# Kernel tuning notes

Hardware: AMD Instinct MI355X
Metric: run time of the kernel (lower is better)

## Reference

```python
import jax, jax.numpy as jnp
import numpy as np

TEMPERATURE = 0.07
N_ANCHORS = 256
THRESHOLD = 0.1
EPS_VALID = 1e-6


def setup_inputs() -> dict:
    key = jax.random.key(0)
    kf, kp, ka = jax.random.split(key, 3)
    B, N, D, H, W = 8, 4, 256, 48, 64
    HW = H * W
    # channels-first features, as the module's permute branch expects
    features = jax.random.normal(kf, (B, N, D, H, W), dtype=jnp.float32)
    # uniform[0,1) -> all points valid (norm > 1e-6) and NN dists mostly < threshold
    pointmaps = jax.random.uniform(kp, (B, N, H, W, 3), dtype=jnp.float32)
    # deterministic stand-in for torch.randperm(N_i)[:n_anchors], one per (view pair, batch)
    keys = jax.random.split(ka, (N - 1) * B)
    perm = jax.vmap(lambda k: jax.random.permutation(k, HW)[:N_ANCHORS])(keys)
    anchor_idx = perm.reshape(N - 1, B, N_ANCHORS).astype(jnp.int32)
    return {"features": features, "pointmaps": pointmaps, "anchor_idx": anchor_idx}


def _l2norm(x):
    # F.normalize(dim=-1) semantics
    return x / jnp.clip(jnp.linalg.norm(x, axis=-1, keepdims=True), 1e-12)


def _pair_loss(fi, fj, pi, pj, vi, vj, aidx):
    # fi, fj: [HW, D]; pi, pj: [HW, 3]; vi, vj: [HW] bool; aidx: [A]
    a_pts = pi[aidx]                                   # [A, 3]
    a_feats = fi[aidx]                                 # [A, D]
    # cdist(anchor_pts, pts_j): [A, HW]
    d2 = jnp.sum((a_pts[:, None, :] - pj[None, :, :]) ** 2, axis=-1)
    dists = jnp.sqrt(jnp.maximum(d2, 0.0))
    dists = jnp.where(vj[None, :], dists, jnp.inf)     # invalid j points can't be matched
    pos_idx = jnp.argmin(dists, axis=-1)               # [A]
    min_d = jnp.min(dists, axis=-1)                    # [A]
    valid_a = (min_d < THRESHOLD) & vi[aidx]           # anchor must be valid + matched
    a_n = _l2norm(a_feats)                             # [A, D]
    p_n = _l2norm(fj[pos_idx])                         # [A, D]
    all_n = _l2norm(fj)                                # [HW, D]
    pos_sim = jnp.sum(a_n * p_n, axis=-1) / TEMPERATURE            # [A]
    all_sim = jnp.einsum('ad,jd->aj', a_n, all_n) / TEMPERATURE    # [A, HW]
    all_sim = jnp.where(vj[None, :], all_sim, -jnp.inf)            # mask invalid negatives
    loss_a = -pos_sim + jax.nn.logsumexp(all_sim, axis=-1)         # [A]
    cnt = jnp.sum(valid_a)
    loss_b = jnp.sum(jnp.where(valid_a, loss_a, 0.0)) / jnp.maximum(cnt, 1)
    include = (cnt >= 5) & (jnp.sum(vi) >= 10) & (jnp.sum(vj) >= 10)
    return loss_b, include


def reference(features, pointmaps, anchor_idx):
    if features.shape[-1] != features.shape[-2]:
        features = jnp.transpose(features, (0, 1, 3, 4, 2))  # [B,N,D,H,W] -> [B,N,H,W,D]
    B, N, H, W, D = features.shape
    feats = features.reshape(B, N, H * W, D)
    pts = pointmaps.reshape(B, N, H * W, 3)
    valid = jnp.linalg.norm(pts, axis=-1) > EPS_VALID    # [B, N, HW]
    total = jnp.float32(0.0)
    for v in range(1, N):  # small fixed loop over view pairs (0, v)
        lb, inc = jax.vmap(_pair_loss)(
            feats[:, 0], feats[:, v], pts[:, 0], pts[:, v],
            valid[:, 0], valid[:, v], anchor_idx[v - 1])
        n_inc = jnp.sum(inc)
        pair = jnp.where(n_inc > 0,
                         jnp.sum(jnp.where(inc, lb, 0.0)) / jnp.maximum(n_inc, 1),
                         0.0)
        total = total + pair
    return total / max(N - 1, 1)
```

## Files before the change

### kernel.cpp

```cpp
#include <hip/hip_runtime.h>
#include <math.h>

#define B_ 8
#define N_ 4
#define D_ 256
#define HW_ 3072
#define A_ 256
#define NP_ 3
#define NJT2_ 48
#define NJB_ 96
#define INV_T 14.2857142857142857f
#define LDKH 64

typedef _Float16 half8 __attribute__((ext_vector_type(8)));
typedef _Float16 half2v __attribute__((ext_vector_type(2)));
typedef float f32x4 __attribute__((ext_vector_type(4)));
typedef unsigned uint2v __attribute__((ext_vector_type(2)));

__global__ __launch_bounds__(256) void k_prep_nn(const float* __restrict__ f,
        const float* __restrict__ pts, _Float16* __restrict__ fh,
        float* __restrict__ srn_g,
        unsigned char* __restrict__ valid, int* __restrict__ vcnt_part,
        const int* __restrict__ aidx, int* __restrict__ pos_idx,
        unsigned char* __restrict__ valid_a, int* __restrict__ ticket) {
  __shared__ float ssql[4][8][4];
  int tid = threadIdx.x;

  if (blockIdx.x < 96) {
    int j0 = blockIdx.x * 32;
    int bn = blockIdx.y;
    int n = bn & 3;
    int jq = tid & 7;
    int dr = (tid >> 3) & 15;
    int hh = tid >> 7;

    f32x4 rv[2][4];
#pragma unroll
    for (int dtl = 0; dtl < 2; ++dtl) {
      int dt = 2 * hh + dtl;
      const float* fb = f + ((size_t)bn * D_ + dt * 64 + 4 * dr) * HW_ + j0 + 4 * jq;
      rv[dtl][0] = *(const f32x4*)&fb[0];
      rv[dtl][1] = *(const f32x4*)&fb[HW_];
      rv[dtl][2] = *(const f32x4*)&fb[2 * HW_];
      rv[dtl][3] = *(const f32x4*)&fb[3 * HW_];
    }

#pragma unroll
    for (int dtl = 0; dtl < 2; ++dtl) {
      int dt = 2 * hh + dtl;
      f32x4 r0 = rv[dtl][0], r1 = rv[dtl][1], r2 = rv[dtl][2], r3 = rv[dtl][3];
#pragma unroll
      for (int jj = 0; jj < 4; ++jj) {
        half2v a, b2;
        a[0]  = (_Float16)r0[jj]; a[1]  = (_Float16)r1[jj];
        b2[0] = (_Float16)r2[jj]; b2[1] = (_Float16)r3[jj];
        uint2v w;
        w[0] = __builtin_bit_cast(unsigned, a);
        w[1] = __builtin_bit_cast(unsigned, b2);
        *(uint2v*)&fh[((size_t)bn * HW_ + j0 + 4 * jq + jj) * D_ + dt * 64 + 4 * dr] = w;
      }
    }

    float ssq0 = 0.f, ssq1 = 0.f, ssq2 = 0.f, ssq3 = 0.f;
#pragma unroll
    for (int dtl = 0; dtl < 2; ++dtl) {
      f32x4 r0 = rv[dtl][0], r1 = rv[dtl][1], r2 = rv[dtl][2], r3 = rv[dtl][3];
      ssq0 = fmaf(r0[0], r0[0], fmaf(r1[0], r1[0], fmaf(r2[0], r2[0], fmaf(r3[0], r3[0], ssq0))));
      ssq1 = fmaf(r0[1], r0[1], fmaf(r1[1], r1[1], fmaf(r2[1], r2[1], fmaf(r3[1], r3[1], ssq1))));
      ssq2 = fmaf(r0[2], r0[2], fmaf(r1[2], r1[2], fmaf(r2[2], r2[2], fmaf(r3[2], r3[2], ssq2))));
      ssq3 = fmaf(r0[3], r0[3], fmaf(r1[3], r1[3], fmaf(r2[3], r2[3], fmaf(r3[3], r3[3], ssq3))));
    }
    ssq0 += __shfl_xor(ssq0, 8); ssq0 += __shfl_xor(ssq0, 16); ssq0 += __shfl_xor(ssq0, 32);
    ssq1 += __shfl_xor(ssq1, 8); ssq1 += __shfl_xor(ssq1, 16); ssq1 += __shfl_xor(ssq1, 32);
    ssq2 += __shfl_xor(ssq2, 8); ssq2 += __shfl_xor(ssq2, 16); ssq2 += __shfl_xor(ssq2, 32);
    ssq3 += __shfl_xor(ssq3, 8); ssq3 += __shfl_xor(ssq3, 16); ssq3 += __shfl_xor(ssq3, 32);
    if ((tid & 63) < 8) {
      int w = tid >> 6;
      ssql[w][jq][0] = ssq0; ssql[w][jq][1] = ssq1;
      ssql[w][jq][2] = ssq2; ssql[w][jq][3] = ssq3;
    }
    __syncthreads();
    if (tid < 32) {
      float s = ssql[0][tid >> 2][tid & 3] + ssql[1][tid >> 2][tid & 3]
              + ssql[2][tid >> 2][tid & 3] + ssql[3][tid >> 2][tid & 3];
      float r = 1.f / fmaxf(sqrtf(s), 1e-12f);
      size_t idx = (size_t)bn * HW_ + j0 + tid;
      srn_g[idx] = (n == 0) ? r * INV_T : r;
      const float* p = pts + idx * 3;
      float x = p[0], y = p[1], z = p[2];
      int v = (x * x + y * y + z * z) > 1e-12f ? 1 : 0;
      valid[idx] = (unsigned char)v;
      unsigned long long mask = __ballot(v);
      if (tid == 0) vcnt_part[bn * NJB_ + blockIdx.x] = __popcll(mask);
    }
  } else {
    int gid = (blockIdx.x - 96) * 32 + blockIdx.y;
    if (gid == 0 && tid == 0) *ticket = 0;
    int wave = tid >> 6, lane = tid & 63;
    int agrp = gid & 63;
    int b = (gid >> 6) & 7;
    int p = gid >> 9;
    int a = agrp * 4 + wave;
    int vv = p + 1;
    int col = aidx[(p * B_ + b) * A_ + a];
    const float* pi = pts + ((size_t)(b * N_) * HW_ + col) * 3;
    float ax = pi[0], ay = pi[1], az = pi[2];
    int vi = (ax * ax + ay * ay + az * az) > 1e-12f ? 1 : 0;
    const f32x4* pj4 = (const f32x4*)(pts + (size_t)(b * N_ + vv) * HW_ * 3);
    float best = INFINITY; int bidx = 0x7fffffff;
#pragma unroll 2
    for (int t = 0; t < HW_ / 256; ++t) {
      int jb = t * 256 + lane * 4;
      int base = t * 192 + lane * 3;
      f32x4 q0 = pj4[base + 0];
      f32x4 q1 = pj4[base + 1];
      f32x4 q2 = pj4[base + 2];
      float px[4] = {q0[0], q0[3], q1[2], q2[1]};
      float py[4] = {q0[1], q1[0], q1[3], q2[2]};
      float pz[4] = {q0[2], q1[1], q2[0], q2[3]};
#pragma unroll
      for (int k = 0; k < 4; ++k) {
        float x = px[k], y = py[k], z = pz[k];
        int vj = (x * x + y * y + z * z) > 1e-12f;
        float dx = ax - x, dy = ay - y, dz = az - z;
        float dist = sqrtf(dx * dx + dy * dy + dz * dz);
        int j = jb + k;
        if (vj && (dist < best || (dist == best && j < bidx))) { best = dist; bidx = j; }
      }
    }
#pragma unroll
    for (int o = 32; o > 0; o >>= 1) {
      float ob = __shfl_xor(best, o);
      int oi = __shfl_xor(bidx, o);
      if (ob < best || (ob == best && oi < bidx)) { best = ob; bidx = oi; }
    }
    if (lane == 0) {
      int ai = (p * B_ + b) * A_ + a;
      pos_idx[ai] = (bidx == 0x7fffffff) ? 0 : bidx;
      valid_a[ai] = (best < 0.1f) && vi;
    }
  }
}

#define STAGE_AB(KK, BUF) do {                                                 \
  _Pragma("unroll")                                                            \
  for (int cc = 0; cc < 4; ++cc) {                                             \
    const _Float16* srcA = fA + (size_t)colA[cc] * D_ + (KK) * 64 + gsw * 8;   \
    __builtin_amdgcn_global_load_lds(                                          \
        (const __attribute__((address_space(1))) void*)srcA,                   \
        (__attribute__((address_space(3))) void*)&As[BUF][(wid * 32 + cc * 8) * LDKH], \
        16, 0, 0);                                                             \
  }                                                                            \
  _Pragma("unroll")                                                            \
  for (int cc = 0; cc < 4; ++cc) {                                             \
    const _Float16* srcB = fB + (size_t)rowB[cc] * D_ + (KK) * 64 + gsw * 8;   \
    __builtin_amdgcn_global_load_lds(                                          \
        (const __attribute__((address_space(1))) void*)srcB,                   \
        (__attribute__((address_space(3))) void*)&Bs[BUF][(wid * 32 + cc * 8) * LDKH], \
        16, 0, 0);                                                             \
  }                                                                            \
} while (0)

__global__ __launch_bounds__(256) void k_gemm(const _Float16* __restrict__ fh,
    const float* __restrict__ srn_g, const int* __restrict__ aidx,
    const unsigned char* __restrict__ valid, const int* __restrict__ pos_idx,
    float* __restrict__ possim, float2* __restrict__ partials) {
  __shared__ __align__(16) char smem[65536];
  _Float16 (*As)[128 * LDKH] = reinterpret_cast<_Float16 (*)[128 * LDKH]>(smem);
  _Float16 (*Bs)[128 * LDKH] = reinterpret_cast<_Float16 (*)[128 * LDKH]>(smem + 32768);
  float (*scr)[132] = reinterpret_cast<float (*)[132]>(smem);

  int jt = blockIdx.x;
  int pbm = blockIdx.y;
  int pb = pbm >> 1, mt = pbm & 1;
  int b = pb & 7, p = pb >> 3, v = p + 1;
  int tid = threadIdx.x;
  int wid = tid >> 6, lane = tid & 63;
  int wr = wid >> 1, wc = wid & 1;
  int j0 = jt * 128;
  const _Float16* fA = fh + (size_t)(b * N_) * HW_ * D_;
  const _Float16* fB = fh + (size_t)(b * N_ + v) * HW_ * D_;

  int rl = lane >> 3;
  int gl = lane & 7;
  int gsw = gl ^ rl;
  int colA[4];
#pragma unroll
  for (int c = 0; c < 4; ++c)
    colA[c] = aidx[(p * B_ + b) * A_ + mt * 128 + wid * 32 + c * 8 + rl];
  int rowB[4];
#pragma unroll
  for (int c = 0; c < 4; ++c) rowB[c] = j0 + wid * 32 + c * 8 + rl;

  f32x4 acc[4][4];
#pragma unroll
  for (int m = 0; m < 4; ++m)
#pragma unroll
    for (int n = 0; n < 4; ++n) acc[m][n] = (f32x4)0.f;

  int kg = lane >> 4;
  int fr = lane & 15;

  STAGE_AB(0, 0);
  __syncthreads();

#pragma unroll
  for (int kk = 0; kk < 4; ++kk) {
    const int cur = kk & 1;
    if (kk < 3) STAGE_AB(kk + 1, cur ^ 1);
#pragma unroll
    for (int s = 0; s < 2; ++s) {
      half8 af[4], bf[4];
      int G = s * 4 + kg;
#pragma unroll
      for (int m = 0; m < 4; ++m) {
        int row = wr * 64 + m * 16 + fr;
        af[m] = *(half8*)&As[cur][row * LDKH + ((G ^ (row & 7)) << 3)];
      }
#pragma unroll
      for (int n = 0; n < 4; ++n) {
        int row = wc * 64 + n * 16 + fr;
        bf[n] = *(half8*)&Bs[cur][row * LDKH + ((G ^ (row & 7)) << 3)];
      }
      __builtin_amdgcn_s_setprio(1);
#pragma unroll
      for (int m = 0; m < 4; ++m)
#pragma unroll
        for (int n = 0; n < 4; ++n)
          acc[m][n] = __builtin_amdgcn_mfma_f32_16x16x32_f16(af[m], bf[n], acc[m][n], 0, 0, 0);
      __builtin_amdgcn_s_setprio(0);
    }
    if (kk < 3) __syncthreads();
  }

  __syncthreads();

  int vrow = b * N_ + v;
  int a_loc = tid >> 1, h = tid & 1;
  int aig = pb * A_ + mt * 128 + a_loc;
  int pidx = pos_idx[aig];
  int colAe = aidx[(p * B_ + b) * A_ + mt * 128 + a_loc];
  float sA = srn_g[(size_t)(b * N_) * HW_ + colAe];

#pragma unroll
  for (int pss = 0; pss < 2; ++pss) {
    if (wc == pss) {
#pragma unroll
      for (int m = 0; m < 4; ++m)
#pragma unroll
        for (int n = 0; n < 4; ++n)
          *(f32x4*)&scr[n * 16 + fr][wr * 64 + m * 16 + kg * 4] = acc[m][n];
    }
    __syncthreads();
    int jbase = j0 + pss * 64 + h * 32;
    const unsigned* vp = (const unsigned*)(valid + (size_t)vrow * HW_ + jbase);
    unsigned vw[8];
#pragma unroll
    for (int w = 0; w < 8; ++w) vw[w] = vp[w];
    float sB[32];
#pragma unroll
    for (int q4 = 0; q4 < 8; ++q4)
      *(f32x4*)&sB[q4 * 4] = *(const f32x4*)&srn_g[(size_t)vrow * HW_ + jbase + q4 * 4];
    float vv[32];
#pragma unroll
    for (int jj = 0; jj < 32; ++jj)
      vv[jj] = scr[h * 32 + jj][a_loc] * sA * sB[jj];
    float mx = -INFINITY;
#pragma unroll
    for (int jj = 0; jj < 32; ++jj) {
      if ((vw[jj >> 2] >> ((jj & 3) * 8)) & 0xff) mx = fmaxf(mx, vv[jj]);
      if (jbase + jj == pidx) possim[aig] = vv[jj];
    }
    float S = 0.f;
#pragma unroll
    for (int jj = 0; jj < 32; ++jj) {
      if ((vw[jj >> 2] >> ((jj & 3) * 8)) & 0xff) S += __expf(vv[jj] - mx);
    }
    float am = fmaxf(mx, __shfl_xor(mx, 1));
    float Ss = (mx == am) ? S : S * __expf(mx - am);
    Ss += __shfl_xor(Ss, 1);
    if (h == 0) partials[(size_t)aig * NJT2_ + (jt * 2 + pss)] = make_float2(am, Ss);
    __syncthreads();
  }
}

__global__ __launch_bounds__(1024) void k_merge(const float2* __restrict__ partials,
    const float* __restrict__ possim, const unsigned char* __restrict__ valid_a,
    const int* __restrict__ vcnt_part, float* __restrict__ lossb,
    int* __restrict__ incb, int* __restrict__ ticket, float* __restrict__ out) {
  int pb = blockIdx.x;
  int b = pb & 7, p = pb >> 3;
  int tid = threadIdx.x;
  int a = tid >> 2, q = tid & 3;
  int ai = pb * A_ + a;

  __shared__ float ss[16]; __shared__ int sc[16];
  __shared__ int v0c, vvc;
  if (tid == 0) { v0c = 0; vvc = 0; }
  __syncthreads();
  if (tid < NJB_) atomicAdd(&v0c, vcnt_part[(b * N_ + 0) * NJB_ + tid]);
  else if (tid < 2 * NJB_) atomicAdd(&vvc, vcnt_part[(b * N_ + p + 1) * NJB_ + (tid - NJB_)]);

  const float4* pt = (const float4*)partials + (size_t)ai * 24 + q * 6;
  float4 vv4[6];
#pragma unroll
  for (int i = 0; i < 6; ++i) vv4[i] = pt[i];
  float mx = -INFINITY;
#pragma unroll
  for (int i = 0; i < 6; ++i) { mx = fmaxf(mx, vv4[i].x); mx = fmaxf(mx, vv4[i].z); }
  float S = 0.f;
  if (mx != -INFINITY) {
#pragma unroll
    for (int i = 0; i < 6; ++i) {
      S += vv4[i].y * __expf(vv4[i].x - mx);
      S += vv4[i].w * __expf(vv4[i].z - mx);
    }
  }
  float am = mx;
#pragma unroll
  for (int o = 1; o < 4; o <<= 1) am = fmaxf(am, __shfl_xor(am, o));
  float Sg = S * ((mx == am) ? 1.f : __expf(mx - am));
#pragma unroll
  for (int o = 1; o < 4; o <<= 1) Sg += __shfl_xor(Sg, o);

  float contrib = 0.f; int cnt = 0;
  if (q == 0) {
    float lse = (am == -INFINITY) ? -INFINITY : am + logf(Sg);
    if (valid_a[ai]) { contrib = lse - possim[ai]; cnt = 1; }
  }
#pragma unroll
  for (int o = 4; o < 64; o <<= 1) {
    contrib += __shfl_xor(contrib, o);
    cnt += __shfl_xor(cnt, o);
  }
  if ((tid & 63) == 0) { ss[tid >> 6] = contrib; sc[tid >> 6] = cnt; }
  __syncthreads();
  if (tid == 0) {
    float s = 0.f; int c = 0;
#pragma unroll
    for (int i = 0; i < 16; ++i) { s += ss[i]; c += sc[i]; }
    float lb = s / (float)(c > 1 ? c : 1);
    int inc = (c >= 5) && (v0c >= 10) && (vvc >= 10);
    lossb[pb] = lb;
    incb[pb] = inc;
    __threadfence();
    int old = atomicAdd(ticket, 1);
    if (old == NP_ * B_ - 1) {
      __threadfence();
      float total = 0.f;
      for (int pp = 0; pp < NP_; ++pp) {
        float sacc = 0.f; int n = 0;
        for (int bb = 0; bb < B_; ++bb)
          if (incb[pp * B_ + bb]) { sacc += lossb[pp * B_ + bb]; ++n; }
        total += (n > 0) ? sacc / (float)n : 0.f;
      }
      out[0] = total / (float)NP_;
    }
  }
}

extern "C" void kernel_launch(void* const* d_in, const int* in_sizes, int n_in,
                              void* d_out, int out_size, void* d_ws, size_t ws_size,
                              hipStream_t stream) {
  const float* f   = (const float*)d_in[0];
  const float* pts = (const float*)d_in[1];
  const int* aidx  = (const int*)d_in[2];
  float* out = (float*)d_out;

  char* ws = (char*)d_ws;
  _Float16* fh          = (_Float16*)(ws);
  unsigned char* valid  = (unsigned char*)(ws + 50331648);
  int* pos_idx          = (int*)(ws + 50429952);
  unsigned char* valid_a= (unsigned char*)(ws + 50454528);
  float* possim         = (float*)(ws + 50460672);
  float* lossb          = (float*)(ws + 50485248);
  int* incb             = (int*)(ws + 50485376);
  float2* partials      = (float2*)(ws + 50485504);
  int* vcnt_part        = (int*)(ws + 52844800);
  int* ticket           = (int*)(ws + 52857088);
  float* srn_g          = (float*)(ws + 52857216);

  k_prep_nn<<<dim3(144, 32), 256, 0, stream>>>(f, pts, fh, srn_g, valid, vcnt_part,
                                               aidx, pos_idx, valid_a, ticket);
  k_gemm<<<dim3(24, NP_ * B_ * 2), 256, 0, stream>>>(fh, srn_g, aidx, valid, pos_idx,
                                                     possim, partials);
  k_merge<<<NP_ * B_, 1024, 0, stream>>>(partials, possim, valid_a, vcnt_part, lossb, incb, ticket, out);
}
```

Before: 89.03 us.

## Transpose features through swizzled LDS slab with async loads and atomic norm accumulation

The prep kernel now stages a 64-channel by 256-pixel fp32 tile into LDS with direct global-to-LDS loads, using an XOR swizzle. Each thread then reads one pixel's column, converts it to fp16 and writes 128-byte contiguous rows of the transposed feature buffer. Squared norms are accumulated across channel blocks with float atomics into a zeroed buffer, and the reciprocal norm is computed later in the GEMM epilogue. This aims for wider, more coalesced stores and fewer blocks. The cost is an extra memset, atomics, and per-element sqrt/reciprocal work in the GEMM epilogue.

```diff
diff --git a/kernel.cpp b/kernel.cpp
--- a/kernel.cpp
+++ b/kernel.cpp
@@ -8,93 +8,75 @@
 #define A_ 256
 #define NP_ 3
 #define NJT2_ 48
-#define NJB_ 96
+#define NJB_ 12
 #define INV_T 14.2857142857142857f
 #define LDKH 64
 
 typedef _Float16 half8 __attribute__((ext_vector_type(8)));
 typedef _Float16 half2v __attribute__((ext_vector_type(2)));
 typedef float f32x4 __attribute__((ext_vector_type(4)));
-typedef unsigned uint2v __attribute__((ext_vector_type(2)));
+typedef unsigned uint4v __attribute__((ext_vector_type(4)));
 
 __global__ __launch_bounds__(256) void k_prep_nn(const float* __restrict__ f,
         const float* __restrict__ pts, _Float16* __restrict__ fh,
-        float* __restrict__ srn_g,
+        float* __restrict__ ssq_g,
         unsigned char* __restrict__ valid, int* __restrict__ vcnt_part,
         const int* __restrict__ aidx, int* __restrict__ pos_idx,
         unsigned char* __restrict__ valid_a, int* __restrict__ ticket) {
-  __shared__ float ssql[4][8][4];
+  __shared__ __align__(16) float slab[64 * 256];
   int tid = threadIdx.x;
 
-  if (blockIdx.x < 96) {
-    int j0 = blockIdx.x * 32;
+  if (blockIdx.x < 48) {
+    int jt = blockIdx.x >> 2;
+    int dt = blockIdx.x & 3;
     int bn = blockIdx.y;
-    int n = bn & 3;
-    int jq = tid & 7;
-    int dr = (tid >> 3) & 15;
-    int hh = tid >> 7;
-
-    f32x4 rv[2][4];
-#pragma unroll
-    for (int dtl = 0; dtl < 2; ++dtl) {
-      int dt = 2 * hh + dtl;
-      const float* fb = f + ((size_t)bn * D_ + dt * 64 + 4 * dr) * HW_ + j0 + 4 * jq;
-      rv[dtl][0] = *(const f32x4*)&fb[0];
-      rv[dtl][1] = *(const f32x4*)&fb[HW_];
-      rv[dtl][2] = *(const f32x4*)&fb[2 * HW_];
-      rv[dtl][3] = *(const f32x4*)&fb[3 * HW_];
-    }
-
-#pragma unroll
-    for (int dtl = 0; dtl < 2; ++dtl) {
-      int dt = 2 * hh + dtl;
-      f32x4 r0 = rv[dtl][0], r1 = rv[dtl][1], r2 = rv[dtl][2], r3 = rv[dtl][3];
-#pragma unroll
-      for (int jj = 0; jj < 4; ++jj) {
-        half2v a, b2;
-        a[0]  = (_Float16)r0[jj]; a[1]  = (_Float16)r1[jj];
-        b2[0] = (_Float16)r2[jj]; b2[1] = (_Float16)r3[jj];
-        uint2v w;
-        w[0] = __builtin_bit_cast(unsigned, a);
-        w[1] = __builtin_bit_cast(unsigned, b2);
-        *(uint2v*)&fh[((size_t)bn * HW_ + j0 + 4 * jq + jj) * D_ + dt * 64 + 4 * dr] = w;
-      }
-    }
-
-    float ssq0 = 0.f, ssq1 = 0.f, ssq2 = 0.f, ssq3 = 0.f;
-#pragma unroll
-    for (int dtl = 0; dtl < 2; ++dtl) {
-      f32x4 r0 = rv[dtl][0], r1 = rv[dtl][1], r2 = rv[dtl][2], r3 = rv[dtl][3];
-      ssq0 = fmaf(r0[0], r0[0], fmaf(r1[0], r1[0], fmaf(r2[0], r2[0], fmaf(r3[0], r3[0], ssq0))));
-      ssq1 = fmaf(r0[1], r0[1], fmaf(r1[1], r1[1], fmaf(r2[1], r2[1], fmaf(r3[1], r3[1], ssq1))));
-      ssq2 = fmaf(r0[2], r0[2], fmaf(r1[2], r1[2], fmaf(r2[2], r2[2], fmaf(r3[2], r3[2], ssq2))));
-      ssq3 = fmaf(r0[3], r0[3], fmaf(r1[3], r1[3], fmaf(r2[3], r2[3], fmaf(r3[3], r3[3], ssq3))));
-    }
-    ssq0 += __shfl_xor(ssq0, 8); ssq0 += __shfl_xor(ssq0, 16); ssq0 += __shfl_xor(ssq0, 32);
-    ssq1 += __shfl_xor(ssq1, 8); ssq1 += __shfl_xor(ssq1, 16); ssq1 += __shfl_xor(ssq1, 32);
-    ssq2 += __shfl_xor(ssq2, 8); ssq2 += __shfl_xor(ssq2, 16); ssq2 += __shfl_xor(ssq2, 32);
-    ssq3 += __shfl_xor(ssq3, 8); ssq3 += __shfl_xor(ssq3, 16); ssq3 += __shfl_xor(ssq3, 32);
-    if ((tid & 63) < 8) {
-      int w = tid >> 6;
-      ssql[w][jq][0] = ssq0; ssql[w][jq][1] = ssq1;
-      ssql[w][jq][2] = ssq2; ssql[w][jq][3] = ssq3;
+    int wid = tid >> 6, lane = tid & 63;
+
+#pragma unroll
+    for (int i = 0; i < 16; ++i) {
+      int r = wid * 16 + i;
+      const float* src = f + ((size_t)bn * D_ + dt * 64 + r) * HW_
+                         + jt * 256 + ((lane ^ (r & 7)) << 2);
+      __builtin_amdgcn_global_load_lds(
+          (const __attribute__((address_space(1))) void*)src,
+          (__attribute__((address_space(3))) void*)&slab[r * 256],
+          16, 0, 0);
     }
     __syncthreads();
-    if (tid < 32) {
-      float s = ssql[0][tid >> 2][tid & 3] + ssql[1][tid >> 2][tid & 3]
-              + ssql[2][tid >> 2][tid & 3] + ssql[3][tid >> 2][tid & 3];
-      float r = 1.f / fmaxf(sqrtf(s), 1e-12f);
-      size_t idx = (size_t)bn * HW_ + j0 + tid;
-      srn_g[idx] = (n == 0) ? r * INV_T : r;
-      const float* p = pts + idx * 3;
+
+    int j = tid;
+    int gj = j >> 2, jo = j & 3;
+    float ssq = 0.f;
+    unsigned pack[32];
+#pragma unroll
+    for (int r2 = 0; r2 < 32; ++r2) {
+      int r0 = 2 * r2, r1 = 2 * r2 + 1;
+      float v0 = slab[r0 * 256 + ((gj ^ (r0 & 7)) << 2) + jo];
+      float v1 = slab[r1 * 256 + ((gj ^ (r1 & 7)) << 2) + jo];
+      ssq = fmaf(v0, v0, ssq);
+      ssq = fmaf(v1, v1, ssq);
+      half2v h;
+      h[0] = (_Float16)v0; h[1] = (_Float16)v1;
+      pack[r2] = __builtin_bit_cast(unsigned, h);
+    }
+    size_t jg = (size_t)bn * HW_ + jt * 256 + j;
+    atomicAdd(&ssq_g[jg], ssq);
+    unsigned* outw = (unsigned*)fh;
+    size_t rb = jg * (D_ / 2) + dt * 32;
+#pragma unroll
+    for (int q = 0; q < 8; ++q)
+      *(uint4v*)&outw[rb + q * 4] = *(uint4v*)&pack[q * 4];
+
+    if (dt == 0) {
+      const float* p = pts + jg * 3;
       float x = p[0], y = p[1], z = p[2];
       int v = (x * x + y * y + z * z) > 1e-12f ? 1 : 0;
-      valid[idx] = (unsigned char)v;
+      valid[jg] = (unsigned char)v;
       unsigned long long mask = __ballot(v);
-      if (tid == 0) vcnt_part[bn * NJB_ + blockIdx.x] = __popcll(mask);
+      if (lane == 0) atomicAdd(&vcnt_part[bn * NJB_ + jt], __popcll(mask));
     }
   } else {
-    int gid = (blockIdx.x - 96) * 32 + blockIdx.y;
+    int gid = (blockIdx.x - 48) * 32 + blockIdx.y;
     if (gid == 0 && tid == 0) *ticket = 0;
     int wave = tid >> 6, lane = tid & 63;
     int agrp = gid & 63;
@@ -124,8 +106,8 @@
         int vj = (x * x + y * y + z * z) > 1e-12f;
         float dx = ax - x, dy = ay - y, dz = az - z;
         float dist = sqrtf(dx * dx + dy * dy + dz * dz);
-        int j = jb + k;
-        if (vj && (dist < best || (dist == best && j < bidx))) { best = dist; bidx = j; }
+        int jx = jb + k;
+        if (vj && (dist < best || (dist == best && jx < bidx))) { best = dist; bidx = jx; }
       }
     }
 #pragma unroll
@@ -162,7 +144,7 @@
 } while (0)
 
 __global__ __launch_bounds__(256) void k_gemm(const _Float16* __restrict__ fh,
-    const float* __restrict__ srn_g, const int* __restrict__ aidx,
+    const float* __restrict__ ssq_g, const int* __restrict__ aidx,
     const unsigned char* __restrict__ valid, const int* __restrict__ pos_idx,
     float* __restrict__ possim, float2* __restrict__ partials) {
   __shared__ __align__(16) char smem[65536];
@@ -240,7 +222,8 @@
   int aig = pb * A_ + mt * 128 + a_loc;
   int pidx = pos_idx[aig];
   int colAe = aidx[(p * B_ + b) * A_ + mt * 128 + a_loc];
-  float sA = srn_g[(size_t)(b * N_) * HW_ + colAe];
+  float sqa = ssq_g[(size_t)(b * N_) * HW_ + colAe];
+  float sA = (1.f / fmaxf(sqrtf(sqa), 1e-12f)) * INV_T;
 
 #pragma unroll
   for (int pss = 0; pss < 2; ++pss) {
@@ -259,8 +242,12 @@
     for (int w = 0; w < 8; ++w) vw[w] = vp[w];
     float sB[32];
 #pragma unroll
-    for (int q4 = 0; q4 < 8; ++q4)
-      *(f32x4*)&sB[q4 * 4] = *(const f32x4*)&srn_g[(size_t)vrow * HW_ + jbase + q4 * 4];
+    for (int q4 = 0; q4 < 8; ++q4) {
+      f32x4 sq = *(const f32x4*)&ssq_g[(size_t)vrow * HW_ + jbase + q4 * 4];
+#pragma unroll
+      for (int e = 0; e < 4; ++e)
+        sB[q4 * 4 + e] = 1.f / fmaxf(sqrtf(sq[e]), 1e-12f);
+    }
     float vv[32];
 #pragma unroll
     for (int jj = 0; jj < 32; ++jj)
@@ -376,13 +363,15 @@
   float* lossb          = (float*)(ws + 50485248);
   int* incb             = (int*)(ws + 50485376);
   float2* partials      = (float2*)(ws + 50485504);
-  int* vcnt_part        = (int*)(ws + 52844800);
-  int* ticket           = (int*)(ws + 52857088);
-  float* srn_g          = (float*)(ws + 52857216);
-
-  k_prep_nn<<<dim3(144, 32), 256, 0, stream>>>(f, pts, fh, srn_g, valid, vcnt_part,
-                                               aidx, pos_idx, valid_a, ticket);
-  k_gemm<<<dim3(24, NP_ * B_ * 2), 256, 0, stream>>>(fh, srn_g, aidx, valid, pos_idx,
+  float* ssq_g          = (float*)(ws + 52844800);
+  int* vcnt_part        = (int*)(ws + 53238016);
+  int* ticket           = (int*)(ws + 53239552);
+
+  hipMemsetAsync(ws + 52844800, 0, 394752, stream);
+
+  k_prep_nn<<<dim3(96, 32), 256, 0, stream>>>(f, pts, fh, ssq_g, valid, vcnt_part,
+                                              aidx, pos_idx, valid_a, ticket);
+  k_gemm<<<dim3(24, NP_ * B_ * 2), 256, 0, stream>>>(fh, ssq_g, aidx, valid, pos_idx,
                                                      possim, partials);
   k_merge<<<NP_ * B_, 1024, 0, stream>>>(partials, possim, valid_a, vcnt_part, lossb, incb, ticket, out);
 }
```

Measured after the change: 120.2 us. +35.0%, slower.
